# Kernel tuning notes

Measured on AMD Instinct MI355X. Metric: run time of the kernel, lower is better.

The kernel has to match this reference:

```python
import jax, jax.numpy as jnp
import numpy as np

B, T, D = 2, 2048, 1024
H = 16
DH = D // H
SCALE = DH ** -0.5


def setup_inputs() -> dict:
    key = jax.random.key(0)
    ks = jax.random.split(key, 10)
    s = lambda fan_in: 1.0 / np.sqrt(fan_in)
    # weights stored (in, out) so y = x @ W + b (torch Linear transposed)
    return {
        "x": jax.random.normal(ks[0], (B, T, D), dtype=jnp.float32),
        "Wqkv0": jax.random.uniform(ks[1], (D, 3 * D), jnp.float32, -s(D), s(D)),
        "bqkv0": jax.random.uniform(ks[2], (3 * D,), jnp.float32, -s(D), s(D)),
        "Wqkv1": jax.random.uniform(ks[3], (D, 3 * D), jnp.float32, -s(D), s(D)),
        "bqkv1": jax.random.uniform(ks[4], (3 * D,), jnp.float32, -s(D), s(D)),
        "Wg": jax.random.uniform(ks[5], (2 * D, D), jnp.float32, -s(2 * D), s(2 * D)),
        "bg": jax.random.uniform(ks[6], (D,), jnp.float32, -s(2 * D), s(2 * D)),
        "Wo": jax.random.uniform(ks[7], (D, D), jnp.float32, -s(D), s(D)),
        "bo": jax.random.uniform(ks[8], (D,), jnp.float32, -s(D), s(D)),
    }


def _attend(x, Wqkv, bqkv):
    # x: [B,T,D] -> qkv: [B,T,3,H,DH]
    qkv = (x @ Wqkv + bqkv).reshape(B, T, 3, H, DH)
    q, k, v = qkv[:, :, 0], qkv[:, :, 1], qkv[:, :, 2]  # [B,T,H,DH]
    scores = jnp.einsum("bqhd,bkhd->bhqk", q, k) * SCALE
    causal = jnp.tril(jnp.ones((T, T), dtype=bool))
    scores = jnp.where(causal, scores, jnp.finfo(scores.dtype).min)
    attn = jax.nn.softmax(scores, axis=-1)  # dropout is identity in eval mode
    out = jnp.einsum("bhqk,bkhd->bqhd", attn, v)
    return out.reshape(B, T, D)


def reference(x, Wqkv0, bqkv0, Wqkv1, bqkv1, Wg, bg, Wo, bo):
    pred = _attend(x, Wqkv0, bqkv0)
    output = pred
    cumulative = pred
    # n_rounds = 2 -> one correction round
    residual = x - cumulative
    correction = _attend(residual, Wqkv1, bqkv1)
    gate = jax.nn.sigmoid(jnp.concatenate([cumulative, correction], axis=-1) @ Wg + bg)
    gated = gate * correction
    output = output + gated
    return output @ Wo + bo
```

## Files before the change

kernel.cpp:

```cpp
#include <hip/hip_runtime.h>
#include <hip/hip_bf16.h>


typedef __bf16 bf16x8 __attribute__((ext_vector_type(8)));
typedef float f32x4 __attribute__((ext_vector_type(4)));

__device__ __forceinline__ unsigned short f2bf(float f) {
  union { __hip_bfloat16 h; unsigned short u; } cv;
  cv.h = __float2bfloat16(f);
  return cv.u;
}

#define GLD16(gp, lp) __builtin_amdgcn_global_load_lds(                      \
    (const __attribute__((address_space(1))) void*)(gp),                     \
    (__attribute__((address_space(3))) void*)(lp), 16, 0, 0)

__global__ __launch_bounds__(256) void transpose_cast(
    const float* __restrict__ in, __hip_bfloat16* __restrict__ out, int R, int C) {
  __shared__ float t[32][33];
  int bx = blockIdx.x * 32, by = blockIdx.y * 32;
  int tx = threadIdx.x, ty = threadIdx.y;
#pragma unroll
  for (int i = 0; i < 32; i += 8)
    t[ty + i][tx] = in[(size_t)(by + ty + i) * C + bx + tx];
  __syncthreads();
#pragma unroll
  for (int i = 0; i < 32; i += 8)
    out[(size_t)(bx + ty + i) * R + by + tx] = __float2bfloat16(t[tx][ty + i]);
}

__global__ __launch_bounds__(256) void cast_f32_bf16(
    const float* __restrict__ in, __hip_bfloat16* __restrict__ out) {
  size_t e = ((size_t)blockIdx.x * blockDim.x + threadIdx.x) * 4;
  float4 v = *(const float4*)(in + e);
  ushort4 o;
  o.x = f2bf(v.x); o.y = f2bf(v.y); o.z = f2bf(v.z); o.w = f2bf(v.w);
  *(ushort4*)((unsigned short*)out + e) = o;
}

__global__ __launch_bounds__(256) void resid_cast(
    const float* __restrict__ x, const float* __restrict__ pred,
    __hip_bfloat16* __restrict__ catb, __hip_bfloat16* __restrict__ residb) {
  size_t e = ((size_t)blockIdx.x * blockDim.x + threadIdx.x) * 4;
  float4 xv = *(const float4*)(x + e);
  float4 pv = *(const float4*)(pred + e);
  size_t row = e >> 10, col = e & 1023;
  ushort4 pb, rb;
  pb.x = f2bf(pv.x); pb.y = f2bf(pv.y); pb.z = f2bf(pv.z); pb.w = f2bf(pv.w);
  rb.x = f2bf(xv.x - pv.x); rb.y = f2bf(xv.y - pv.y);
  rb.z = f2bf(xv.z - pv.z); rb.w = f2bf(xv.w - pv.w);
  *(ushort4*)((unsigned short*)catb + row * 2048 + col) = pb;
  *(ushort4*)((unsigned short*)residb + e) = rb;
}

__global__ __launch_bounds__(256) void corr_cast(
    const float* __restrict__ corr, __hip_bfloat16* __restrict__ catb) {
  size_t e = ((size_t)blockIdx.x * blockDim.x + threadIdx.x) * 4;
  float4 v = *(const float4*)(corr + e);
  size_t row = e >> 10, col = e & 1023;
  ushort4 o;
  o.x = f2bf(v.x); o.y = f2bf(v.y); o.z = f2bf(v.z); o.w = f2bf(v.w);
  *(ushort4*)((unsigned short*)catb + row * 2048 + 1024 + col) = o;
}

template <int EPI>
__global__ __launch_bounds__(256) void gemm_bf16(
    const __hip_bfloat16* __restrict__ A, const __hip_bfloat16* __restrict__ Bt,
    const float* __restrict__ bias, void* __restrict__ outp,
    const float* __restrict__ aux0, const float* __restrict__ aux1,
    int M, int N, int K) {
  __shared__ __hip_bfloat16 As[2][128 * 32];
  __shared__ __hip_bfloat16 Bs[2][128 * 32];
  const int tid = threadIdx.x;
  const int lane = tid & 63, wid = tid >> 6;
  const int wr = wid >> 1, wc = wid & 1;
  const int lr = lane & 15, lk = (lane >> 4) * 8;
  const size_t brow = (size_t)blockIdx.y * 128, bcol = (size_t)blockIdx.x * 128;
  f32x4 acc[4][4] = {};
#pragma unroll
  for (int r = 0; r < 2; ++r) {
    int c = tid + r * 256;
    GLD16(A + (brow + (size_t)(c >> 2)) * K + (c & 3) * 8, As[0] + c * 8);
    GLD16(Bt + (bcol + (size_t)(c >> 2)) * K + (c & 3) * 8, Bs[0] + c * 8);
  }
  __syncthreads();
  int cur = 0;
  for (int k0 = 0; k0 < K; k0 += 32) {
    const int nxt = cur ^ 1;
    if (k0 + 32 < K) {
#pragma unroll
      for (int r = 0; r < 2; ++r) {
        int c = tid + r * 256;
        GLD16(A + (brow + (size_t)(c >> 2)) * K + k0 + 32 + (c & 3) * 8,
              As[nxt] + c * 8);
        GLD16(Bt + (bcol + (size_t)(c >> 2)) * K + k0 + 32 + (c & 3) * 8,
              Bs[nxt] + c * 8);
      }
    }
    bf16x8 a[4], b[4];
#pragma unroll
    for (int m = 0; m < 4; ++m)
      a[m] = *(const bf16x8*)(As[cur] + (wr * 64 + m * 16 + lr) * 32 + lk);
#pragma unroll
    for (int n = 0; n < 4; ++n)
      b[n] = *(const bf16x8*)(Bs[cur] + (wc * 64 + n * 16 + lr) * 32 + lk);
#pragma unroll
    for (int m = 0; m < 4; ++m)
#pragma unroll
      for (int n = 0; n < 4; ++n)
        acc[m][n] = __builtin_amdgcn_mfma_f32_16x16x32_bf16(a[m], b[n], acc[m][n], 0, 0, 0);
    __syncthreads();
    cur = nxt;
  }
  const int r0 = (lane >> 4) * 4, cn = lane & 15;
#pragma unroll
  for (int m = 0; m < 4; ++m)
#pragma unroll
    for (int n = 0; n < 4; ++n) {
      size_t col = bcol + wc * 64 + n * 16 + cn;
      float bv = bias[col];
#pragma unroll
      for (int j = 0; j < 4; ++j) {
        size_t row = brow + wr * 64 + m * 16 + r0 + j;
        float v = acc[m][n][j] + bv;
        if constexpr (EPI == 0) {
          ((__hip_bfloat16*)outp)[row * N + col] = __float2bfloat16(v);
        } else if constexpr (EPI == 1) {
          float g = 1.0f / (1.0f + __expf(-v));
          float val = g * aux0[row * N + col] + aux1[row * N + col];
          ((__hip_bfloat16*)outp)[row * N + col] = __float2bfloat16(val);
        } else {
          ((float*)outp)[row * N + col] = v;
        }
      }
    }
}

__global__ __launch_bounds__(256) void attn_kernel(
    const __hip_bfloat16* __restrict__ qkv, float* __restrict__ outp) {
  const int b = blockIdx.z, h = blockIdx.y, qtp = blockIdx.x;
  const int qlo = qtp, qhi = 31 - qtp;
  const int q0lo = qlo * 64, q0hi = qhi * 64;
  __shared__ __hip_bfloat16 ks[2][64 * 64];
  __shared__ __hip_bfloat16 vts[2][64 * 64];
  __shared__ __hip_bfloat16 qps[8192];
  const int tid = threadIdx.x, lane = tid & 63, w = tid >> 6;
  const int lr = lane & 15, lg = lane >> 4;
  const int sw = lr & 7;
  const size_t rs = 3072;
  const __hip_bfloat16* qbh = qkv + ((size_t)b * 2048 + q0hi) * rs + h * 64;
  const __hip_bfloat16* qbl = qkv + ((size_t)b * 2048 + q0lo) * rs + h * 64;
  const __hip_bfloat16* kb = qkv + (size_t)b * 2048 * rs + 1024 + h * 64;
  const __hip_bfloat16* vb = qkv + (size_t)b * 2048 * rs + 2048 + h * 64;

  float4 vreg[2];
#pragma unroll
  for (int r = 0; r < 2; ++r) {
    int c = tid + r * 256, row = c >> 3, p = c & 7;
    GLD16(qbh + (size_t)row * rs + (p ^ (row & 7)) * 8, qps + c * 8);
    GLD16(qbl + (size_t)row * rs + (p ^ (row & 7)) * 8, qps + 4096 + c * 8);
    GLD16(kb + (size_t)row * rs + (p ^ (row & 7)) * 8, ks[0] + c * 8);
    vreg[r] = *(const float4*)(vb + (size_t)row * rs + p * 8);
  }
  __syncthreads();
  const int qrow = w * 16 + lr;
  const bf16x8 qh0 = *(const bf16x8*)(qps + qrow * 64 + ((lg) ^ (qrow & 7)) * 8);
  const bf16x8 qh1 = *(const bf16x8*)(qps + qrow * 64 + ((4 + lg) ^ (qrow & 7)) * 8);
  const bf16x8 ql0 = *(const bf16x8*)(qps + 4096 + qrow * 64 + ((lg) ^ (qrow & 7)) * 8);
  const bf16x8 ql1 = *(const bf16x8*)(qps + 4096 + qrow * 64 + ((4 + lg) ^ (qrow & 7)) * 8);
#pragma unroll
  for (int r = 0; r < 2; ++r) {
    int c = tid + r * 256, row = c >> 3, seg = c & 7;
    const __hip_bfloat16* e8 = (const __hip_bfloat16*)&vreg[r];
#pragma unroll
    for (int i = 0; i < 8; ++i)
      vts[0][(seg * 8 + i) * 64 + (((row >> 3) ^ i ^ seg)) * 8 + (row & 7)] = e8[i];
  }
  __syncthreads();

  __hip_bfloat16* psh = qps + w * 1024;
  __hip_bfloat16* psl = qps + 4096 + w * 1024;
  float m_hi = -1e30f, l_hi = 0.f, m_lo = -1e30f, l_lo = 0.f;
  f32x4 o_hi[4] = {}, o_lo[4] = {};
  int cur = 0;

  auto process = [&](const bf16x8& qa0, const bf16x8& qa1, bool diag,
                     float& m_run, float& l_run, f32x4* o, __hip_bfloat16* psw) {
    f32x4 s4[4] = {};
#pragma unroll
    for (int n = 0; n < 4; ++n) {
      const int kr = n * 16 + lr;
      bf16x8 k0f = *(const bf16x8*)(ks[cur] + kr * 64 + ((lg) ^ sw) * 8);
      bf16x8 k1f = *(const bf16x8*)(ks[cur] + kr * 64 + ((4 + lg) ^ sw) * 8);
      s4[n] = __builtin_amdgcn_mfma_f32_16x16x32_bf16(k0f, qa0, s4[n], 0, 0, 0);
      s4[n] = __builtin_amdgcn_mfma_f32_16x16x32_bf16(k1f, qa1, s4[n], 0, 0, 0);
    }
    float p[4][4];
    float mloc = -1e30f;
#pragma unroll
    for (int n = 0; n < 4; ++n)
#pragma unroll
      for (int j = 0; j < 4; ++j) {
        float v = s4[n][j] * 0.125f;
        if (diag && (n * 16 + lg * 4 + j) > (w * 16 + lr)) v = -1e30f;
        p[n][j] = v;
        mloc = fmaxf(mloc, v);
      }
    mloc = fmaxf(mloc, __shfl_xor(mloc, 16));
    mloc = fmaxf(mloc, __shfl_xor(mloc, 32));
    const float mn = fmaxf(m_run, mloc);
    const float sc = __expf(m_run - mn);
    m_run = mn;
    float ls = 0.f;
#pragma unroll
    for (int n = 0; n < 4; ++n)
#pragma unroll
      for (int j = 0; j < 4; ++j) { p[n][j] = __expf(p[n][j] - mn); ls += p[n][j]; }
    ls += __shfl_xor(ls, 16);
    ls += __shfl_xor(ls, 32);
    l_run = l_run * sc + ls;
    float scb[4];
#pragma unroll
    for (int j = 0; j < 4; ++j) scb[j] = __shfl(sc, lg * 4 + j);
#pragma unroll
    for (int n = 0; n < 4; ++n)
#pragma unroll
      for (int j = 0; j < 4; ++j) o[n][j] *= scb[j];
#pragma unroll
    for (int n = 0; n < 4; ++n)
#pragma unroll
      for (int j = 0; j < 4; ++j)
        psw[lr * 64 + ((n * 2 + (lg >> 1)) ^ sw) * 8 + (lg & 1) * 4 + j] =
            __float2bfloat16(p[n][j]);
    bf16x8 pa0 = *(const bf16x8*)(&psw[lr * 64 + ((lg) ^ sw) * 8]);
    bf16x8 pa1 = *(const bf16x8*)(&psw[lr * 64 + ((4 + lg) ^ sw) * 8]);
#pragma unroll
    for (int n = 0; n < 4; ++n) {
      const int vdh = n * 16 + lr;
      const int swv = (vdh & 7) ^ ((vdh >> 3) & 7);
      bf16x8 v0f = *(const bf16x8*)(vts[cur] + vdh * 64 + ((lg) ^ swv) * 8);
      bf16x8 v1f = *(const bf16x8*)(vts[cur] + vdh * 64 + ((4 + lg) ^ swv) * 8);
      o[n] = __builtin_amdgcn_mfma_f32_16x16x32_bf16(pa0, v0f, o[n], 0, 0, 0);
      o[n] = __builtin_amdgcn_mfma_f32_16x16x32_bf16(pa1, v1f, o[n], 0, 0, 0);
    }
  };

  for (int kvt = 0; kvt <= qhi; ++kvt) {
    const int nxt = cur ^ 1;
    const bool pf = (kvt < qhi);
    if (pf) {
      const int kv1 = (kvt + 1) * 64;
#pragma unroll
      for (int r = 0; r < 2; ++r) {
        int c = tid + r * 256, row = c >> 3, p = c & 7;
        GLD16(kb + (size_t)(kv1 + row) * rs + (p ^ (row & 7)) * 8, ks[nxt] + c * 8);
        vreg[r] = *(const float4*)(vb + (size_t)(kv1 + row) * rs + p * 8);
      }
    }
    process(qh0, qh1, kvt == qhi, m_hi, l_hi, o_hi, psh);
    if (kvt <= qlo) process(ql0, ql1, kvt == qlo, m_lo, l_lo, o_lo, psl);
    if (pf) {
#pragma unroll
      for (int r = 0; r < 2; ++r) {
        int c = tid + r * 256, row = c >> 3, seg = c & 7;
        const __hip_bfloat16* e8 = (const __hip_bfloat16*)&vreg[r];
#pragma unroll
        for (int i = 0; i < 8; ++i)
          vts[nxt][(seg * 8 + i) * 64 + (((row >> 3) ^ i ^ seg)) * 8 + (row & 7)] = e8[i];
      }
    }
    __syncthreads();
    cur = nxt;
  }
  const float linv_h = 1.0f / l_hi, linv_l = 1.0f / l_lo;
#pragma unroll
  for (int j = 0; j < 4; ++j) {
    const float lih = __shfl(linv_h, lg * 4 + j);
    const float lil = __shfl(linv_l, lg * 4 + j);
    size_t rowh = (size_t)b * 2048 + q0hi + w * 16 + lg * 4 + j;
    size_t rowl = (size_t)b * 2048 + q0lo + w * 16 + lg * 4 + j;
#pragma unroll
    for (int n = 0; n < 4; ++n) {
      outp[rowh * 1024 + h * 64 + n * 16 + lr] = o_hi[n][j] * lih;
      outp[rowl * 1024 + h * 64 + n * 16 + lr] = o_lo[n][j] * lil;
    }
  }
}

extern "C" void kernel_launch(void* const* d_in, const int* in_sizes, int n_in,
                              void* d_out, int out_size, void* d_ws, size_t ws_size,
                              hipStream_t stream) {
  const float* x     = (const float*)d_in[0];
  const float* Wqkv0 = (const float*)d_in[1];
  const float* bqkv0 = (const float*)d_in[2];
  const float* Wqkv1 = (const float*)d_in[3];
  const float* bqkv1 = (const float*)d_in[4];
  const float* Wg    = (const float*)d_in[5];
  const float* bg    = (const float*)d_in[6];
  const float* Wo    = (const float*)d_in[7];
  const float* bo    = (const float*)d_in[8];
  float* out = (float*)d_out;

  char* ws = (char*)d_ws;
  __hip_bfloat16* xb   = (__hip_bfloat16*)(ws);
  __hip_bfloat16* qkv  = (__hip_bfloat16*)(ws + 8388608);
  float*          pred = (float*)(ws + 33554432);
  float*          corr = (float*)(ws + 50331648);
  __hip_bfloat16* catb = (__hip_bfloat16*)(ws + 67108864);
  __hip_bfloat16* Wt0  = (__hip_bfloat16*)(ws + 83886080);
  __hip_bfloat16* Wt1  = (__hip_bfloat16*)(ws + 90177536);
  __hip_bfloat16* Wgt  = (__hip_bfloat16*)(ws + 96468992);
  __hip_bfloat16* Wot  = (__hip_bfloat16*)(ws + 100663296);

  dim3 tb(32, 8);
  transpose_cast<<<dim3(3072 / 32, 1024 / 32), tb, 0, stream>>>(Wqkv0, Wt0, 1024, 3072);
  transpose_cast<<<dim3(3072 / 32, 1024 / 32), tb, 0, stream>>>(Wqkv1, Wt1, 1024, 3072);
  transpose_cast<<<dim3(1024 / 32, 2048 / 32), tb, 0, stream>>>(Wg, Wgt, 2048, 1024);
  transpose_cast<<<dim3(1024 / 32, 1024 / 32), tb, 0, stream>>>(Wo, Wot, 1024, 1024);
  cast_f32_bf16<<<4096, 256, 0, stream>>>(x, xb);

  gemm_bf16<0><<<dim3(24, 32), 256, 0, stream>>>(xb, Wt0, bqkv0, (void*)qkv,
                                                 nullptr, nullptr, 4096, 3072, 1024);
  attn_kernel<<<dim3(16, 16, 2), 256, 0, stream>>>(qkv, pred);
  resid_cast<<<4096, 256, 0, stream>>>(x, pred, catb, xb);
  gemm_bf16<0><<<dim3(24, 32), 256, 0, stream>>>(xb, Wt1, bqkv1, (void*)qkv,
                                                 nullptr, nullptr, 4096, 3072, 1024);
  attn_kernel<<<dim3(16, 16, 2), 256, 0, stream>>>(qkv, corr);
  corr_cast<<<4096, 256, 0, stream>>>(corr, catb);
  gemm_bf16<1><<<dim3(8, 32), 256, 0, stream>>>(catb, Wgt, bg, (void*)xb,
                                                corr, pred, 4096, 1024, 2048);
  gemm_bf16<2><<<dim3(8, 32), 256, 0, stream>>>(xb, Wot, bo, (void*)out,
                                                nullptr, nullptr, 4096, 1024, 1024);
}
```

Baseline: 309.3 us.

## Use 256x256 triple-buffered GEMM for QKV, fuse bf16 cast into attention, pack V transpose

Replaces the 128x128 double-buffered GEMM for both QKV projections with a 256x256 tile, 512-thread, triple-buffered kernel using explicit vmcnt waits, which raises operand reuse per tile. The attention kernel now also writes its output as bf16 straight into the concatenated gate input, so the separate corr_cast kernel and the pred cast inside resid_cast go away. The V transpose into shared memory now packs two bf16 values per 32-bit store instead of scalar 16-bit stores. The costs are more registers and LDS per block and a grid of only 192 blocks for the QKV GEMM, which may leave some compute units idle.

```diff
diff --git a/kernel.cpp b/kernel.cpp
--- a/kernel.cpp
+++ b/kernel.cpp
@@ -40,27 +40,14 @@
 
 __global__ __launch_bounds__(256) void resid_cast(
     const float* __restrict__ x, const float* __restrict__ pred,
-    __hip_bfloat16* __restrict__ catb, __hip_bfloat16* __restrict__ residb) {
+    __hip_bfloat16* __restrict__ residb) {
   size_t e = ((size_t)blockIdx.x * blockDim.x + threadIdx.x) * 4;
   float4 xv = *(const float4*)(x + e);
   float4 pv = *(const float4*)(pred + e);
-  size_t row = e >> 10, col = e & 1023;
-  ushort4 pb, rb;
-  pb.x = f2bf(pv.x); pb.y = f2bf(pv.y); pb.z = f2bf(pv.z); pb.w = f2bf(pv.w);
+  ushort4 rb;
   rb.x = f2bf(xv.x - pv.x); rb.y = f2bf(xv.y - pv.y);
   rb.z = f2bf(xv.z - pv.z); rb.w = f2bf(xv.w - pv.w);
-  *(ushort4*)((unsigned short*)catb + row * 2048 + col) = pb;
   *(ushort4*)((unsigned short*)residb + e) = rb;
-}
-
-__global__ __launch_bounds__(256) void corr_cast(
-    const float* __restrict__ corr, __hip_bfloat16* __restrict__ catb) {
-  size_t e = ((size_t)blockIdx.x * blockDim.x + threadIdx.x) * 4;
-  float4 v = *(const float4*)(corr + e);
-  size_t row = e >> 10, col = e & 1023;
-  ushort4 o;
-  o.x = f2bf(v.x); o.y = f2bf(v.y); o.z = f2bf(v.z); o.w = f2bf(v.w);
-  *(ushort4*)((unsigned short*)catb + row * 2048 + 1024 + col) = o;
 }
 
 template <int EPI>
@@ -123,21 +110,96 @@
       for (int j = 0; j < 4; ++j) {
         size_t row = brow + wr * 64 + m * 16 + r0 + j;
         float v = acc[m][n][j] + bv;
-        if constexpr (EPI == 0) {
-          ((__hip_bfloat16*)outp)[row * N + col] = __float2bfloat16(v);
-        } else if constexpr (EPI == 1) {
+        if constexpr (EPI == 1) {
           float g = 1.0f / (1.0f + __expf(-v));
           float val = g * aux0[row * N + col] + aux1[row * N + col];
           ((__hip_bfloat16*)outp)[row * N + col] = __float2bfloat16(val);
+        } else if constexpr (EPI == 2) {
+          ((float*)outp)[row * N + col] = v;
         } else {
-          ((float*)outp)[row * N + col] = v;
+          ((__hip_bfloat16*)outp)[row * N + col] = __float2bfloat16(v);
         }
       }
     }
 }
 
+__global__ __launch_bounds__(512) void gemm256_bf16(
+    const __hip_bfloat16* __restrict__ A, const __hip_bfloat16* __restrict__ Bt,
+    const float* __restrict__ bias, __hip_bfloat16* __restrict__ outp,
+    int M, int N, int K) {
+  __shared__ __hip_bfloat16 As[3][256 * 32];
+  __shared__ __hip_bfloat16 Bs[3][256 * 32];
+  const int tid = threadIdx.x;
+  const int lane = tid & 63, wid = tid >> 6;
+  const int wr = wid >> 2, wc = wid & 3;
+  const int lr = lane & 15, lg = lane >> 4;
+  const size_t brow = (size_t)blockIdx.y * 256, bcol = (size_t)blockIdx.x * 256;
+  f32x4 acc[8][4] = {};
+
+  auto stage = [&](int t, int buf) {
+#pragma unroll
+    for (int r = 0; r < 2; ++r) {
+      int c = tid + r * 512, row = c >> 2, slot = c & 3;
+      GLD16(A + (brow + (size_t)row) * K + t * 32 + ((slot ^ (row & 3)) * 8),
+            As[buf] + c * 8);
+      GLD16(Bt + (bcol + (size_t)row) * K + t * 32 + ((slot ^ (row & 3)) * 8),
+            Bs[buf] + c * 8);
+    }
+  };
+
+  const int nT = K >> 5;
+  stage(0, 0);
+  stage(1, 1);
+  asm volatile("s_waitcnt vmcnt(4)" ::: "memory");
+  __builtin_amdgcn_s_barrier();
+  int cur = 0;
+  for (int t = 0; t < nT; ++t) {
+    const int b2 = (cur + 2 >= 3) ? cur - 1 : cur + 2;
+    if (t + 2 < nT) stage(t + 2, b2);
+    const __hip_bfloat16* Ab = As[cur];
+    const __hip_bfloat16* Bb = Bs[cur];
+    bf16x8 a[8], b[4];
+#pragma unroll
+    for (int m = 0; m < 8; ++m) {
+      const int row = wr * 128 + m * 16 + lr;
+      a[m] = *(const bf16x8*)(Ab + row * 32 + ((lg ^ (row & 3)) * 8));
+    }
+#pragma unroll
+    for (int n = 0; n < 4; ++n) {
+      const int row = wc * 64 + n * 16 + lr;
+      b[n] = *(const bf16x8*)(Bb + row * 32 + ((lg ^ (row & 3)) * 8));
+    }
+#pragma unroll
+    for (int m = 0; m < 8; ++m)
+#pragma unroll
+      for (int n = 0; n < 4; ++n)
+        acc[m][n] = __builtin_amdgcn_mfma_f32_16x16x32_bf16(a[m], b[n], acc[m][n], 0, 0, 0);
+    if (t + 2 < nT) {
+      asm volatile("s_waitcnt vmcnt(4)" ::: "memory");
+    } else {
+      asm volatile("s_waitcnt vmcnt(0)" ::: "memory");
+    }
+    __builtin_amdgcn_s_barrier();
+    cur = (cur + 1 >= 3) ? 0 : cur + 1;
+  }
+  const int r0 = (lane >> 4) * 4, cn = lane & 15;
+#pragma unroll
+  for (int m = 0; m < 8; ++m)
+#pragma unroll
+    for (int n = 0; n < 4; ++n) {
+      size_t col = bcol + wc * 64 + n * 16 + cn;
+      float bv = bias[col];
+#pragma unroll
+      for (int j = 0; j < 4; ++j) {
+        size_t row = brow + wr * 128 + m * 16 + r0 + j;
+        outp[row * N + col] = __float2bfloat16(acc[m][n][j] + bv);
+      }
+    }
+}
+
 __global__ __launch_bounds__(256) void attn_kernel(
-    const __hip_bfloat16* __restrict__ qkv, float* __restrict__ outp) {
+    const __hip_bfloat16* __restrict__ qkv, float* __restrict__ outp,
+    __hip_bfloat16* __restrict__ outb, int ob_off) {
   const int b = blockIdx.z, h = blockIdx.y, qtp = blockIdx.x;
   const int qlo = qtp, qhi = 31 - qtp;
   const int q0lo = qlo * 64, q0hi = qhi * 64;
@@ -153,28 +215,33 @@
   const __hip_bfloat16* kb = qkv + (size_t)b * 2048 * rs + 1024 + h * 64;
   const __hip_bfloat16* vb = qkv + (size_t)b * 2048 * rs + 2048 + h * 64;
 
-  float4 vreg[2];
+  const int vrow2 = tid >> 3, vseg = tid & 7;
+  float4 vr0, vr1;
 #pragma unroll
   for (int r = 0; r < 2; ++r) {
     int c = tid + r * 256, row = c >> 3, p = c & 7;
     GLD16(qbh + (size_t)row * rs + (p ^ (row & 7)) * 8, qps + c * 8);
     GLD16(qbl + (size_t)row * rs + (p ^ (row & 7)) * 8, qps + 4096 + c * 8);
     GLD16(kb + (size_t)row * rs + (p ^ (row & 7)) * 8, ks[0] + c * 8);
-    vreg[r] = *(const float4*)(vb + (size_t)row * rs + p * 8);
-  }
+  }
+  vr0 = *(const float4*)(vb + (size_t)(2 * vrow2) * rs + vseg * 8);
+  vr1 = *(const float4*)(vb + (size_t)(2 * vrow2 + 1) * rs + vseg * 8);
   __syncthreads();
   const int qrow = w * 16 + lr;
   const bf16x8 qh0 = *(const bf16x8*)(qps + qrow * 64 + ((lg) ^ (qrow & 7)) * 8);
   const bf16x8 qh1 = *(const bf16x8*)(qps + qrow * 64 + ((4 + lg) ^ (qrow & 7)) * 8);
   const bf16x8 ql0 = *(const bf16x8*)(qps + 4096 + qrow * 64 + ((lg) ^ (qrow & 7)) * 8);
   const bf16x8 ql1 = *(const bf16x8*)(qps + 4096 + qrow * 64 + ((4 + lg) ^ (qrow & 7)) * 8);
-#pragma unroll
-  for (int r = 0; r < 2; ++r) {
-    int c = tid + r * 256, row = c >> 3, seg = c & 7;
-    const __hip_bfloat16* e8 = (const __hip_bfloat16*)&vreg[r];
-#pragma unroll
-    for (int i = 0; i < 8; ++i)
-      vts[0][(seg * 8 + i) * 64 + (((row >> 3) ^ i ^ seg)) * 8 + (row & 7)] = e8[i];
+  {
+    const unsigned short* u0 = (const unsigned short*)&vr0;
+    const unsigned short* u1 = (const unsigned short*)&vr1;
+#pragma unroll
+    for (int i = 0; i < 8; ++i) {
+      const int dh = vseg * 8 + i;
+      const int phys = (vrow2 >> 2) ^ (dh & 7) ^ ((dh >> 3) & 7);
+      unsigned int pk = (unsigned int)u0[i] | ((unsigned int)u1[i] << 16);
+      *(unsigned int*)(vts[0] + dh * 64 + phys * 8 + 2 * (vrow2 & 3)) = pk;
+    }
   }
   __syncthreads();
 
@@ -254,19 +321,21 @@
       for (int r = 0; r < 2; ++r) {
         int c = tid + r * 256, row = c >> 3, p = c & 7;
         GLD16(kb + (size_t)(kv1 + row) * rs + (p ^ (row & 7)) * 8, ks[nxt] + c * 8);
-        vreg[r] = *(const float4*)(vb + (size_t)(kv1 + row) * rs + p * 8);
-      }
+      }
+      vr0 = *(const float4*)(vb + (size_t)(kv1 + 2 * vrow2) * rs + vseg * 8);
+      vr1 = *(const float4*)(vb + (size_t)(kv1 + 2 * vrow2 + 1) * rs + vseg * 8);
     }
     process(qh0, qh1, kvt == qhi, m_hi, l_hi, o_hi, psh);
     if (kvt <= qlo) process(ql0, ql1, kvt == qlo, m_lo, l_lo, o_lo, psl);
     if (pf) {
-#pragma unroll
-      for (int r = 0; r < 2; ++r) {
-        int c = tid + r * 256, row = c >> 3, seg = c & 7;
-        const __hip_bfloat16* e8 = (const __hip_bfloat16*)&vreg[r];
-#pragma unroll
-        for (int i = 0; i < 8; ++i)
-          vts[nxt][(seg * 8 + i) * 64 + (((row >> 3) ^ i ^ seg)) * 8 + (row & 7)] = e8[i];
+      const unsigned short* u0 = (const unsigned short*)&vr0;
+      const unsigned short* u1 = (const unsigned short*)&vr1;
+#pragma unroll
+      for (int i = 0; i < 8; ++i) {
+        const int dh = vseg * 8 + i;
+        const int phys = (vrow2 >> 2) ^ (dh & 7) ^ ((dh >> 3) & 7);
+        unsigned int pk = (unsigned int)u0[i] | ((unsigned int)u1[i] << 16);
+        *(unsigned int*)(vts[nxt] + dh * 64 + phys * 8 + 2 * (vrow2 & 3)) = pk;
       }
     }
     __syncthreads();
@@ -281,8 +350,11 @@
     size_t rowl = (size_t)b * 2048 + q0lo + w * 16 + lg * 4 + j;
 #pragma unroll
     for (int n = 0; n < 4; ++n) {
-      outp[rowh * 1024 + h * 64 + n * 16 + lr] = o_hi[n][j] * lih;
-      outp[rowl * 1024 + h * 64 + n * 16 + lr] = o_lo[n][j] * lil;
+      float vh = o_hi[n][j] * lih, vl = o_lo[n][j] * lil;
+      outp[rowh * 1024 + h * 64 + n * 16 + lr] = vh;
+      outp[rowl * 1024 + h * 64 + n * 16 + lr] = vl;
+      outb[rowh * 2048 + ob_off + h * 64 + n * 16 + lr] = __float2bfloat16(vh);
+      outb[rowl * 2048 + ob_off + h * 64 + n * 16 + lr] = __float2bfloat16(vl);
     }
   }
 }
@@ -319,14 +391,11 @@
   transpose_cast<<<dim3(1024 / 32, 1024 / 32), tb, 0, stream>>>(Wo, Wot, 1024, 1024);
   cast_f32_bf16<<<4096, 256, 0, stream>>>(x, xb);
 
-  gemm_bf16<0><<<dim3(24, 32), 256, 0, stream>>>(xb, Wt0, bqkv0, (void*)qkv,
-                                                 nullptr, nullptr, 4096, 3072, 1024);
-  attn_kernel<<<dim3(16, 16, 2), 256, 0, stream>>>(qkv, pred);
-  resid_cast<<<4096, 256, 0, stream>>>(x, pred, catb, xb);
-  gemm_bf16<0><<<dim3(24, 32), 256, 0, stream>>>(xb, Wt1, bqkv1, (void*)qkv,
-                                                 nullptr, nullptr, 4096, 3072, 1024);
-  attn_kernel<<<dim3(16, 16, 2), 256, 0, stream>>>(qkv, corr);
-  corr_cast<<<4096, 256, 0, stream>>>(corr, catb);
+  gemm256_bf16<<<dim3(12, 16), 512, 0, stream>>>(xb, Wt0, bqkv0, qkv, 4096, 3072, 1024);
+  attn_kernel<<<dim3(16, 16, 2), 256, 0, stream>>>(qkv, pred, catb, 0);
+  resid_cast<<<4096, 256, 0, stream>>>(x, pred, xb);
+  gemm256_bf16<<<dim3(12, 16), 512, 0, stream>>>(xb, Wt1, bqkv1, qkv, 4096, 3072, 1024);
+  attn_kernel<<<dim3(16, 16, 2), 256, 0, stream>>>(qkv, corr, catb, 1024);
   gemm_bf16<1><<<dim3(8, 32), 256, 0, stream>>>(catb, Wgt, bg, (void*)xb,
                                                 corr, pred, 4096, 1024, 2048);
   gemm_bf16<2><<<dim3(8, 32), 256, 0, stream>>>(xb, Wot, bo, (void*)out,
```

New measurement: 327.1 us. 1.06x slower.
